# Kernel tuning notes

Hardware: AMD Instinct MI355X
Metric: run time of the kernel (lower is better)

The kernel has to match this reference:

```python
import jax, jax.numpy as jnp
import numpy as np

NEG_SLOPE = 0.2  # PyG GATConv default


def gat_conv(x, edge_index, W, att_src, att_dst, bias):
    """PyG-style GATConv with default add_self_loops=True.
    x: [N, Fin], W: [Fin, H*C], att_src/att_dst: [H, C], bias: [H*C].
    Returns [N, H*C] (heads concatenated).
    """
    N = x.shape[0]
    H, C = att_src.shape
    h = (x @ W).reshape(N, H, C)              # per-head projected features
    loops = jnp.arange(N, dtype=edge_index.dtype)
    src = jnp.concatenate([edge_index[0], loops])  # message sources j
    dst = jnp.concatenate([edge_index[1], loops])  # aggregation targets i
    a_src = (h * att_src).sum(-1)             # [N, H]
    a_dst = (h * att_dst).sum(-1)             # [N, H]
    e = jax.nn.leaky_relu(a_src[src] + a_dst[dst], NEG_SLOPE)  # [E, H]
    # segment softmax over incoming edges of each dst node
    m = jax.ops.segment_max(e, dst, num_segments=N)            # [N, H]
    ex = jnp.exp(e - m[dst])
    denom = jax.ops.segment_sum(ex, dst, num_segments=N)       # [N, H]
    alpha = ex / denom[dst]                                    # [E, H]
    out = jax.ops.segment_sum(alpha[:, :, None] * h[src], dst, num_segments=N)  # [N, H, C]
    return out.reshape(N, H * C) + bias


def setup_inputs() -> dict:
    key = jax.random.key(0)
    ks = jax.random.split(key, 10)
    N, E, Fin, Hid, Heads, Out = 50000, 800000, 256, 64, 2, 64
    x = jax.random.normal(ks[0], (N, Fin), dtype=jnp.float32)
    edge_index = jax.random.randint(ks[1], (2, E), 0, N, dtype=jnp.int32)
    s1 = 1.0 / np.sqrt(Fin)
    s2 = 1.0 / np.sqrt(Hid * Heads)
    return {
        "x": x,
        "edge_index": edge_index,
        "W1": jax.random.normal(ks[2], (Fin, Heads * Hid), dtype=jnp.float32) * s1,
        "att_src1": jax.random.normal(ks[3], (Heads, Hid), dtype=jnp.float32) * s1,
        "att_dst1": jax.random.normal(ks[4], (Heads, Hid), dtype=jnp.float32) * s1,
        "b1": jnp.zeros((Heads * Hid,), dtype=jnp.float32),
        "W2": jax.random.normal(ks[5], (Heads * Hid, Out), dtype=jnp.float32) * s2,
        "att_src2": jax.random.normal(ks[6], (1, Out), dtype=jnp.float32) * s2,
        "att_dst2": jax.random.normal(ks[7], (1, Out), dtype=jnp.float32) * s2,
        "b2": jnp.zeros((Out,), dtype=jnp.float32),
    }


def reference(x, edge_index, W1, att_src1, att_dst1, b1, W2, att_src2, att_dst2, b2):
    h = gat_conv(x, edge_index, W1, att_src1, att_dst1, b1)
    h = jax.nn.relu(h)
    return gat_conv(h, edge_index, W2, att_src2, att_dst2, b2)
```

## Files before the change

kernel.cpp:

```cpp
#include <hip/hip_runtime.h>
#include <math.h>

#define NEG_SLOPE 0.2f

typedef unsigned short u16;
typedef unsigned int u32;
typedef _Float16 f16;
typedef __attribute__((ext_vector_type(8))) _Float16 f16x8;
typedef __attribute__((ext_vector_type(4))) float f32x4;

__device__ __forceinline__ float lrelu(float x) { return x > 0.f ? x : NEG_SLOPE * x; }
__device__ __forceinline__ u16 f2h(float f) { f16 h = (f16)f; return __builtin_bit_cast(u16, h); }
__device__ __forceinline__ float2 hp2f(u32 v) {
  union { u32 u; f16 h[2]; } c; c.u = v;
  return make_float2((float)c.h[0], (float)c.h[1]);
}
__device__ __forceinline__ u32 pk2h(float a, float b) {
  auto h = __builtin_amdgcn_cvt_pkrtz(a, b);
  return __builtin_bit_cast(u32, h);
}
__device__ __forceinline__ uint4 relu8h(uint4 v) {
  union { uint4 u; f16 h[8]; } c; c.u = v;
#pragma unroll
  for (int i = 0; i < 8; ++i) c.h[i] = (c.h[i] > (f16)0.f) ? c.h[i] : (f16)0.f;
  return c.u;
}

__global__ void prep_k(const float* __restrict__ W1, const float* __restrict__ W2,
                       u16* __restrict__ W1t, u16* __restrict__ W2t,
                       int* __restrict__ deg, int N) {
  int i = blockIdx.x * 256 + threadIdx.x;
  if (i < 128 * 256) { int n = i >> 8, k = i & 255; W1t[i] = f2h(W1[k * 128 + n]); }
  if (i < 64 * 128)  { int n = i >> 7, k = i & 127; W2t[i] = f2h(W2[k * 64 + n]); }
  if (i < N) deg[i] = 0;
}

__global__ void hist_k(const int* __restrict__ ei, int* __restrict__ deg,
                       int* __restrict__ rank, int E, int NE) {
  int e = blockIdx.x * blockDim.x + threadIdx.x;
  if (e >= NE) return;
  int dst = (e < E) ? ei[E + e] : e - E;
  rank[e] = atomicAdd(&deg[dst], 1);
}

__global__ void scatter_k(const int* __restrict__ ei, const int* __restrict__ rank,
                          u16* __restrict__ srcs2, int E, int NE) {
  int e = blockIdx.x * blockDim.x + threadIdx.x;
  if (e >= NE) return;
  int src, dst;
  if (e < E) { src = ei[e]; dst = ei[E + e]; } else { src = e - E; dst = src; }
  int r = rank[e];
  if (r < 64) srcs2[(size_t)dst * 64 + r] = (u16)src;
}

__global__ __launch_bounds__(256) void gemm1_mfma_k(const float* __restrict__ A,
                                                    const u16* __restrict__ Bt,
                                                    const float* __restrict__ asv,
                                                    const float* __restrict__ adv,
                                                    u16* __restrict__ C,
                                                    float* __restrict__ aS,
                                                    float* __restrict__ aD, int M) {
  __shared__ u16 Ah[64][40];
  __shared__ u16 Bh[128][40];
  const int tid = threadIdx.x;
  const int lane = tid & 63;
  const int wid = tid >> 6;
  const int wm = wid >> 1, wn = wid & 1;
  const int row0 = blockIdx.x * 64;
  const int l15 = lane & 15;
  const int k8 = (lane >> 4) * 8;

  f32x4 acc[2][4];
#pragma unroll
  for (int i = 0; i < 2; ++i)
#pragma unroll
    for (int j = 0; j < 4; ++j) acc[i][j] = (f32x4){0.f, 0.f, 0.f, 0.f};

  const int ar = tid >> 3;
  const int ac = (tid & 7) * 4;
  const int bn = tid >> 1;
  const int bk = (tid & 1) * 16;

  for (int k0 = 0; k0 < 256; k0 += 32) {
#pragma unroll
    for (int p = 0; p < 2; ++p) {
      int rr = ar + p * 32;
      int gr = row0 + rr; gr = gr < M ? gr : M - 1;
      float4 v = *reinterpret_cast<const float4*>(&A[(size_t)gr * 256 + k0 + ac]);
      uint2 w; w.x = pk2h(v.x, v.y); w.y = pk2h(v.z, v.w);
      *reinterpret_cast<uint2*>(&Ah[rr][ac]) = w;
    }
    {
      int4 v = *reinterpret_cast<const int4*>(&Bt[(size_t)bn * 256 + k0 + bk]);
      *reinterpret_cast<int4*>(&Bh[bn][bk]) = v;
      int4 v2 = *reinterpret_cast<const int4*>(&Bt[(size_t)bn * 256 + k0 + bk + 8]);
      *reinterpret_cast<int4*>(&Bh[bn][bk + 8]) = v2;
    }
    __syncthreads();
    f16x8 af[2], bf[4];
#pragma unroll
    for (int mf = 0; mf < 2; ++mf)
      af[mf] = *reinterpret_cast<const f16x8*>(&Ah[wm * 32 + mf * 16 + l15][k8]);
#pragma unroll
    for (int nf = 0; nf < 4; ++nf)
      bf[nf] = *reinterpret_cast<const f16x8*>(&Bh[wn * 64 + nf * 16 + l15][k8]);
#pragma unroll
    for (int mf = 0; mf < 2; ++mf)
#pragma unroll
      for (int nf = 0; nf < 4; ++nf)
        acc[mf][nf] = __builtin_amdgcn_mfma_f32_16x16x32_f16(af[mf], bf[nf], acc[mf][nf], 0, 0, 0);
    __syncthreads();
  }
#pragma unroll
  for (int mf = 0; mf < 2; ++mf)
#pragma unroll
    for (int r = 0; r < 4; ++r) {
      int row = row0 + wm * 32 + mf * 16 + (lane >> 4) * 4 + r;
      if (row < M) {
#pragma unroll
        for (int nf = 0; nf < 4; ++nf)
          C[(size_t)row * 128 + wn * 64 + nf * 16 + l15] = f2h(acc[mf][nf][r]);
      }
    }
  float as_r[4], ad_r[4];
#pragma unroll
  for (int nf = 0; nf < 4; ++nf) {
    as_r[nf] = asv[wn * 64 + nf * 16 + l15];
    ad_r[nf] = adv[wn * 64 + nf * 16 + l15];
  }
#pragma unroll
  for (int mf = 0; mf < 2; ++mf)
#pragma unroll
    for (int r = 0; r < 4; ++r) {
      float s = 0.f, dd = 0.f;
#pragma unroll
      for (int nf = 0; nf < 4; ++nf) {
        s = fmaf(acc[mf][nf][r], as_r[nf], s);
        dd = fmaf(acc[mf][nf][r], ad_r[nf], dd);
      }
#pragma unroll
      for (int o = 1; o < 16; o <<= 1) {
        s += __shfl_xor(s, o);
        dd += __shfl_xor(dd, o);
      }
      int row = row0 + wm * 32 + mf * 16 + (lane >> 4) * 4 + r;
      if (l15 == 0 && row < M) { aS[2 * row + wn] = s; aD[2 * row + wn] = dd; }
    }
}

__global__ __launch_bounds__(256) void gemm2_mfma_k(const u16* __restrict__ A,
                                                    const u16* __restrict__ Bt,
                                                    const float* __restrict__ asv,
                                                    const float* __restrict__ adv,
                                                    u16* __restrict__ C,
                                                    float* __restrict__ aS,
                                                    float* __restrict__ aD, int M) {
  __shared__ u16 Ah[64][40];
  __shared__ u16 Bh[64][40];
  __shared__ float sS[64][2], sD[64][2];
  const int tid = threadIdx.x;
  const int lane = tid & 63;
  const int wid = tid >> 6;
  const int wm = wid >> 1, wn = wid & 1;
  const int row0 = blockIdx.x * 64;
  const int l15 = lane & 15;
  const int k8 = (lane >> 4) * 8;

  f32x4 acc[2][2];
#pragma unroll
  for (int i = 0; i < 2; ++i)
#pragma unroll
    for (int j = 0; j < 2; ++j) acc[i][j] = (f32x4){0.f, 0.f, 0.f, 0.f};

  const int arr = tid >> 2;
  const int acc8 = (tid & 3) * 8;
  const int bn = tid >> 1;
  const int bk = (tid & 1) * 16;

  for (int k0 = 0; k0 < 128; k0 += 32) {
    {
      int gr = row0 + arr; gr = gr < M ? gr : M - 1;
      uint4 v = *reinterpret_cast<const uint4*>(&A[(size_t)gr * 128 + k0 + acc8]);
      *reinterpret_cast<uint4*>(&Ah[arr][acc8]) = relu8h(v);
    }
    if (bn < 64) {
      int4 v = *reinterpret_cast<const int4*>(&Bt[(size_t)bn * 128 + k0 + bk]);
      *reinterpret_cast<int4*>(&Bh[bn][bk]) = v;
      int4 v2 = *reinterpret_cast<const int4*>(&Bt[(size_t)bn * 128 + k0 + bk + 8]);
      *reinterpret_cast<int4*>(&Bh[bn][bk + 8]) = v2;
    }
    __syncthreads();
    f16x8 af[2], bf[2];
#pragma unroll
    for (int mf = 0; mf < 2; ++mf)
      af[mf] = *reinterpret_cast<const f16x8*>(&Ah[wm * 32 + mf * 16 + l15][k8]);
#pragma unroll
    for (int nf = 0; nf < 2; ++nf)
      bf[nf] = *reinterpret_cast<const f16x8*>(&Bh[wn * 32 + nf * 16 + l15][k8]);
#pragma unroll
    for (int mf = 0; mf < 2; ++mf)
#pragma unroll
      for (int nf = 0; nf < 2; ++nf)
        acc[mf][nf] = __builtin_amdgcn_mfma_f32_16x16x32_f16(af[mf], bf[nf], acc[mf][nf], 0, 0, 0);
    __syncthreads();
  }
#pragma unroll
  for (int mf = 0; mf < 2; ++mf)
#pragma unroll
    for (int r = 0; r < 4; ++r) {
      int row = row0 + wm * 32 + mf * 16 + (lane >> 4) * 4 + r;
      if (row < M) {
#pragma unroll
        for (int nf = 0; nf < 2; ++nf)
          C[(size_t)row * 64 + wn * 32 + nf * 16 + l15] = f2h(acc[mf][nf][r]);
      }
    }
  float as_r[2], ad_r[2];
#pragma unroll
  for (int nf = 0; nf < 2; ++nf) {
    as_r[nf] = asv[wn * 32 + nf * 16 + l15];
    ad_r[nf] = adv[wn * 32 + nf * 16 + l15];
  }
#pragma unroll
  for (int mf = 0; mf < 2; ++mf)
#pragma unroll
    for (int r = 0; r < 4; ++r) {
      float s = 0.f, dd = 0.f;
#pragma unroll
      for (int nf = 0; nf < 2; ++nf) {
        s = fmaf(acc[mf][nf][r], as_r[nf], s);
        dd = fmaf(acc[mf][nf][r], ad_r[nf], dd);
      }
#pragma unroll
      for (int o = 1; o < 16; o <<= 1) {
        s += __shfl_xor(s, o);
        dd += __shfl_xor(dd, o);
      }
      int rl = wm * 32 + mf * 16 + (lane >> 4) * 4 + r;
      if (l15 == 0) { sS[rl][wn] = s; sD[rl][wn] = dd; }
    }
  __syncthreads();
  if (tid < 64) {
    int row = row0 + tid;
    if (row < M) {
      aS[row] = sS[tid][0] + sS[tid][1];
      aD[row] = sD[tid][0] + sD[tid][1];
    }
  }
}

__global__ __launch_bounds__(256) void csr_agg1_k(const u16* __restrict__ srcs2,
                                                  const int* __restrict__ degv,
                                                  const float* __restrict__ aS,
                                                  const float* __restrict__ aD,
                                                  const u16* __restrict__ h1,
                                                  const float* __restrict__ b1,
                                                  u16* __restrict__ out1, int N) {
  int d = (blockIdx.x * 256 + threadIdx.x) >> 6;
  if (d >= N) return;
  int lane = threadIdx.x & 63;
  int deg = degv[d]; deg = deg > 64 ? 64 : deg;
  float aD0 = aD[2 * d], aD1 = aD[2 * d + 1];
  const uint4* h1v = reinterpret_cast<const uint4*>(h1);
  int l15 = lane & 15;
  int qw = lane >> 4;
  int head = l15 >> 3;
  float acc[8];
#pragma unroll
  for (int i = 0; i < 8; ++i) acc[i] = 0.f;

  int src = 0;
  float t0 = -1e30f, t1 = -1e30f;
  if (lane < deg) {
    src = srcs2[(size_t)d * 64 + lane];
    float2 sv = *reinterpret_cast<const float2*>(&aS[2 * src]);
    t0 = lrelu(sv.x + aD0); t1 = lrelu(sv.y + aD1);
  }
  float m0 = t0, m1 = t1;
#pragma unroll
  for (int o = 32; o > 0; o >>= 1) {
    m0 = fmaxf(m0, __shfl_xor(m0, o));
    m1 = fmaxf(m1, __shfl_xor(m1, o));
  }
  float w0 = (lane < deg) ? __expf(t0 - m0) : 0.f;
  float w1 = (lane < deg) ? __expf(t1 - m1) : 0.f;
  float sum0 = w0, sum1 = w1;
#pragma unroll
  for (int o = 32; o > 0; o >>= 1) {
    sum0 += __shfl_xor(sum0, o);
    sum1 += __shfl_xor(sum1, o);
  }
  w0 *= (1.f / sum0); w1 *= (1.f / sum1);

  for (int j = 0; j < deg; j += 16) {
    float aa[4]; uint4 v[4];
#pragma unroll
    for (int q = 0; q < 4; ++q) {
      int ee = j + 4 * q + qw;
      int ec = ee < deg ? ee : 0;
      int se = __shfl(src, ec);
      float a0 = __shfl(w0, ec), a1 = __shfl(w1, ec);
      aa[q] = head ? a1 : a0;
      v[q] = make_uint4(0, 0, 0, 0);
      if (ee < deg) v[q] = h1v[(size_t)se * 16 + l15];
    }
#pragma unroll
    for (int q = 0; q < 4; ++q) {
      float2 f;
      f = hp2f(v[q].x); acc[0] = fmaf(aa[q], f.x, acc[0]); acc[1] = fmaf(aa[q], f.y, acc[1]);
      f = hp2f(v[q].y); acc[2] = fmaf(aa[q], f.x, acc[2]); acc[3] = fmaf(aa[q], f.y, acc[3]);
      f = hp2f(v[q].z); acc[4] = fmaf(aa[q], f.x, acc[4]); acc[5] = fmaf(aa[q], f.y, acc[5]);
      f = hp2f(v[q].w); acc[6] = fmaf(aa[q], f.x, acc[6]); acc[7] = fmaf(aa[q], f.y, acc[7]);
    }
  }
#pragma unroll
  for (int i = 0; i < 8; ++i) {
    acc[i] += __shfl_xor(acc[i], 16);
    acc[i] += __shfl_xor(acc[i], 32);
  }
  if (lane < 16) {
    int fb = l15 * 8;
    uint4 o;
    o.x = pk2h(acc[0] + b1[fb + 0], acc[1] + b1[fb + 1]);
    o.y = pk2h(acc[2] + b1[fb + 2], acc[3] + b1[fb + 3]);
    o.z = pk2h(acc[4] + b1[fb + 4], acc[5] + b1[fb + 5]);
    o.w = pk2h(acc[6] + b1[fb + 6], acc[7] + b1[fb + 7]);
    reinterpret_cast<uint4*>(out1)[(size_t)d * 16 + l15] = o;
  }
}

__global__ __launch_bounds__(256) void csr_agg2_k(const u16* __restrict__ srcs2,
                                                  const int* __restrict__ degv,
                                                  const float* __restrict__ aS,
                                                  const float* __restrict__ aD,
                                                  const u16* __restrict__ h2,
                                                  const float* __restrict__ b2,
                                                  float* __restrict__ out, int N) {
  int d = (blockIdx.x * 256 + threadIdx.x) >> 6;
  if (d >= N) return;
  int lane = threadIdx.x & 63;
  int deg = degv[d]; deg = deg > 64 ? 64 : deg;
  float aDd = aD[d];
  const uint4* h2v = reinterpret_cast<const uint4*>(h2);
  int l7 = lane & 7;
  int g = lane >> 3;
  float acc[8];
#pragma unroll
  for (int i = 0; i < 8; ++i) acc[i] = 0.f;

  int src = 0;
  float t = -1e30f;
  if (lane < deg) {
    src = srcs2[(size_t)d * 64 + lane];
    t = lrelu(aS[src] + aDd);
  }
  float m = t;
#pragma unroll
  for (int o = 32; o > 0; o >>= 1) m = fmaxf(m, __shfl_xor(m, o));
  float w = (lane < deg) ? __expf(t - m) : 0.f;
  float sum = w;
#pragma unroll
  for (int o = 32; o > 0; o >>= 1) sum += __shfl_xor(sum, o);
  w *= (1.f / sum);

  for (int j = 0; j < deg; j += 32) {
    float aa[4]; uint4 v[4];
#pragma unroll
    for (int q = 0; q < 4; ++q) {
      int ee = j + 8 * q + g;
      int ec = ee < deg ? ee : 0;
      int se = __shfl(src, ec);
      aa[q] = __shfl(w, ec);
      v[q] = make_uint4(0, 0, 0, 0);
      if (ee < deg) v[q] = h2v[(size_t)se * 8 + l7];
    }
#pragma unroll
    for (int q = 0; q < 4; ++q) {
      float2 f;
      f = hp2f(v[q].x); acc[0] = fmaf(aa[q], f.x, acc[0]); acc[1] = fmaf(aa[q], f.y, acc[1]);
      f = hp2f(v[q].y); acc[2] = fmaf(aa[q], f.x, acc[2]); acc[3] = fmaf(aa[q], f.y, acc[3]);
      f = hp2f(v[q].z); acc[4] = fmaf(aa[q], f.x, acc[4]); acc[5] = fmaf(aa[q], f.y, acc[5]);
      f = hp2f(v[q].w); acc[6] = fmaf(aa[q], f.x, acc[6]); acc[7] = fmaf(aa[q], f.y, acc[7]);
    }
  }
#pragma unroll
  for (int i = 0; i < 8; ++i) {
    acc[i] += __shfl_xor(acc[i], 8);
    acc[i] += __shfl_xor(acc[i], 16);
    acc[i] += __shfl_xor(acc[i], 32);
  }
  if (lane < 8) {
    int fb = l7 * 8;
    float4 o0 = make_float4(acc[0] + b2[fb + 0], acc[1] + b2[fb + 1],
                            acc[2] + b2[fb + 2], acc[3] + b2[fb + 3]);
    float4 o1 = make_float4(acc[4] + b2[fb + 4], acc[5] + b2[fb + 5],
                            acc[6] + b2[fb + 6], acc[7] + b2[fb + 7]);
    *reinterpret_cast<float4*>(&out[(size_t)d * 64 + fb]) = o0;
    *reinterpret_cast<float4*>(&out[(size_t)d * 64 + fb + 4]) = o1;
  }
}

extern "C" void kernel_launch(void* const* d_in, const int* in_sizes, int n_in,
                              void* d_out, int out_size, void* d_ws, size_t ws_size,
                              hipStream_t stream) {
  const float* x   = (const float*)d_in[0];
  const int*   ei  = (const int*)d_in[1];
  const float* W1  = (const float*)d_in[2];
  const float* as1 = (const float*)d_in[3];
  const float* ad1 = (const float*)d_in[4];
  const float* b1  = (const float*)d_in[5];
  const float* W2  = (const float*)d_in[6];
  const float* as2 = (const float*)d_in[7];
  const float* ad2 = (const float*)d_in[8];
  const float* b2  = (const float*)d_in[9];
  float* out = (float*)d_out;

  const int N = in_sizes[0] / 256;
  const int E = in_sizes[1] / 2;
  const int NE = E + N;

  char* ws = (char*)d_ws;
  size_t woff = 0;
  auto take = [&](size_t bytes) -> char* {
    char* p = ws + woff;
    woff += (bytes + 255) & ~(size_t)255;
    return p;
  };
  u16*   h1    = (u16*)take((size_t)N * 128 * 2);
  u16*   out1  = (u16*)take((size_t)N * 128 * 2);
  float* aS1   = (float*)take((size_t)N * 2 * 4);
  float* aD1   = (float*)take((size_t)N * 2 * 4);
  float* aS2   = (float*)take((size_t)N * 4);
  float* aD2   = (float*)take((size_t)N * 4);
  int*   deg   = (int*)take((size_t)N * 4);
  int*   rank  = (int*)take((size_t)NE * 4);
  u16*   srcs2 = (u16*)take((size_t)N * 64 * 2);
  u16*   W1t   = (u16*)take((size_t)128 * 256 * 2);
  u16*   W2t   = (u16*)take((size_t)64 * 128 * 2);
  u16*   h2    = h1;

  const int egrid = (NE + 255) / 256;
  const int wgrid = (N + 3) / 4;
  const int ggrid = (N + 63) / 64;
  const int nb    = (N + 255) / 256;
  const int pgrid = nb > 128 ? nb : 128;

  prep_k<<<pgrid, 256, 0, stream>>>(W1, W2, W1t, W2t, deg, N);
  hist_k<<<egrid, 256, 0, stream>>>(ei, deg, rank, E, NE);
  scatter_k<<<egrid, 256, 0, stream>>>(ei, rank, srcs2, E, NE);

  gemm1_mfma_k<<<ggrid, 256, 0, stream>>>(x, W1t, as1, ad1, h1, aS1, aD1, N);
  csr_agg1_k<<<wgrid, 256, 0, stream>>>(srcs2, deg, aS1, aD1, h1, b1, out1, N);

  gemm2_mfma_k<<<ggrid, 256, 0, stream>>>(out1, W2t, as2, ad2, h2, aS2, aD2, N);
  csr_agg2_k<<<wgrid, 256, 0, stream>>>(srcs2, deg, aS2, aD2, h2, b2, out, N);
}
```

Before: 148.4 us.

## Split layer-1 CSR aggregation into one wavefront per (node, head)

```diff
diff --git a/kernel.cpp b/kernel.cpp
--- a/kernel.cpp
+++ b/kernel.cpp
@@ -256,53 +256,45 @@
                                                   const u16* __restrict__ h1,
                                                   const float* __restrict__ b1,
                                                   u16* __restrict__ out1, int N) {
-  int d = (blockIdx.x * 256 + threadIdx.x) >> 6;
-  if (d >= N) return;
+  int w = (blockIdx.x * 256 + threadIdx.x) >> 6;
+  if (w >= 2 * N) return;
+  int d = w >> 1, head = w & 1;
   int lane = threadIdx.x & 63;
   int deg = degv[d]; deg = deg > 64 ? 64 : deg;
-  float aD0 = aD[2 * d], aD1 = aD[2 * d + 1];
+  float aDh = aD[2 * d + head];
   const uint4* h1v = reinterpret_cast<const uint4*>(h1);
-  int l15 = lane & 15;
-  int qw = lane >> 4;
-  int head = l15 >> 3;
+  int l7 = lane & 7;
+  int g = lane >> 3;
   float acc[8];
 #pragma unroll
   for (int i = 0; i < 8; ++i) acc[i] = 0.f;
 
   int src = 0;
-  float t0 = -1e30f, t1 = -1e30f;
+  float t = -1e30f;
   if (lane < deg) {
     src = srcs2[(size_t)d * 64 + lane];
-    float2 sv = *reinterpret_cast<const float2*>(&aS[2 * src]);
-    t0 = lrelu(sv.x + aD0); t1 = lrelu(sv.y + aD1);
-  }
-  float m0 = t0, m1 = t1;
-#pragma unroll
-  for (int o = 32; o > 0; o >>= 1) {
-    m0 = fmaxf(m0, __shfl_xor(m0, o));
-    m1 = fmaxf(m1, __shfl_xor(m1, o));
-  }
-  float w0 = (lane < deg) ? __expf(t0 - m0) : 0.f;
-  float w1 = (lane < deg) ? __expf(t1 - m1) : 0.f;
-  float sum0 = w0, sum1 = w1;
-#pragma unroll
-  for (int o = 32; o > 0; o >>= 1) {
-    sum0 += __shfl_xor(sum0, o);
-    sum1 += __shfl_xor(sum1, o);
-  }
-  w0 *= (1.f / sum0); w1 *= (1.f / sum1);
-
-  for (int j = 0; j < deg; j += 16) {
+    t = lrelu(aS[2 * src + head] + aDh);
+  }
+  float m = t;
+#pragma unroll
+  for (int o = 32; o > 0; o >>= 1) m = fmaxf(m, __shfl_xor(m, o));
+  float wgt = (lane < deg) ? __expf(t - m) : 0.f;
+  float sum = wgt;
+#pragma unroll
+  for (int o = 32; o > 0; o >>= 1) sum += __shfl_xor(sum, o);
+  wgt *= (1.f / sum);
+
+  const size_t hb = (size_t)head * 8 + l7;
+  for (int j = 0; j < deg; j += 32) {
     float aa[4]; uint4 v[4];
 #pragma unroll
     for (int q = 0; q < 4; ++q) {
-      int ee = j + 4 * q + qw;
+      int ee = j + 8 * q + g;
       int ec = ee < deg ? ee : 0;
       int se = __shfl(src, ec);
-      float a0 = __shfl(w0, ec), a1 = __shfl(w1, ec);
-      aa[q] = head ? a1 : a0;
+      aa[q] = __shfl(wgt, ec);
       v[q] = make_uint4(0, 0, 0, 0);
-      if (ee < deg) v[q] = h1v[(size_t)se * 16 + l15];
+      if (ee < deg) v[q] = h1v[(size_t)se * 16 + hb];
     }
 #pragma unroll
     for (int q = 0; q < 4; ++q) {
@@ -315,17 +307,18 @@
   }
 #pragma unroll
   for (int i = 0; i < 8; ++i) {
+    acc[i] += __shfl_xor(acc[i], 8);
     acc[i] += __shfl_xor(acc[i], 16);
     acc[i] += __shfl_xor(acc[i], 32);
   }
-  if (lane < 16) {
-    int fb = l15 * 8;
+  if (lane < 8) {
+    int fb = head * 64 + l7 * 8;
     uint4 o;
     o.x = pk2h(acc[0] + b1[fb + 0], acc[1] + b1[fb + 1]);
     o.y = pk2h(acc[2] + b1[fb + 2], acc[3] + b1[fb + 3]);
     o.z = pk2h(acc[4] + b1[fb + 4], acc[5] + b1[fb + 5]);
     o.w = pk2h(acc[6] + b1[fb + 6], acc[7] + b1[fb + 7]);
-    reinterpret_cast<uint4*>(out1)[(size_t)d * 16 + l15] = o;
+    reinterpret_cast<uint4*>(out1)[(size_t)d * 16 + head * 8 + l7] = o;
   }
 }
 
@@ -439,19 +432,20 @@
   u16*   W2t   = (u16*)take((size_t)64 * 128 * 2);
   u16*   h2    = h1;
 
-  const int egrid = (NE + 255) / 256;
-  const int wgrid = (N + 3) / 4;
-  const int ggrid = (N + 63) / 64;
-  const int nb    = (N + 255) / 256;
-  const int pgrid = nb > 128 ? nb : 128;
+  const int egrid  = (NE + 255) / 256;
+  const int wgrid1 = (2 * N + 3) / 4;
+  const int wgrid2 = (N + 3) / 4;
+  const int ggrid  = (N + 63) / 64;
+  const int nb     = (N + 255) / 256;
+  const int pgrid  = nb > 128 ? nb : 128;
 
   prep_k<<<pgrid, 256, 0, stream>>>(W1, W2, W1t, W2t, deg, N);
   hist_k<<<egrid, 256, 0, stream>>>(ei, deg, rank, E, NE);
   scatter_k<<<egrid, 256, 0, stream>>>(ei, rank, srcs2, E, NE);
 
   gemm1_mfma_k<<<ggrid, 256, 0, stream>>>(x, W1t, as1, ad1, h1, aS1, aD1, N);
-  csr_agg1_k<<<wgrid, 256, 0, stream>>>(srcs2, deg, aS1, aD1, h1, b1, out1, N);
+  csr_agg1_k<<<wgrid1, 256, 0, stream>>>(srcs2, deg, aS1, aD1, h1, b1, out1, N);
 
   gemm2_mfma_k<<<ggrid, 256, 0, stream>>>(out1, W2t, as2, ad2, h2, aS2, aD2, N);
-  csr_agg2_k<<<wgrid, 256, 0, stream>>>(srcs2, deg, aS2, aD2, h2, b2, out, N);
-}
+  csr_agg2_k<<<wgrid2, 256, 0, stream>>>(srcs2, deg, aS2, aD2, h2, b2, out, N);
+}
```

Measured after the change: 161.2 us. 1.09x slower.
